# Kernel optimization log

Measured on AMD Instinct MI355X. Metric: run time of the kernel, lower is better.

The kernel has to match this reference:

```python
import jax, jax.numpy as jnp
import numpy as np

EPS_DENOM = 1e-8   # matches probs = counts / (numel + 1e-08)
EPS_LOG = 1e-10    # matches log2(probs + 1e-10)


def setup_inputs() -> dict:
    key = jax.random.key(0)
    values = jax.random.normal(key, (256, 262144), dtype=jnp.float32)
    return {"values": values}


def reference(values):
    # Binary quantization: q = (values > 0). Per batch row, histogram over {0,1}.
    # count1 = number of positives, count0 = N - count1. The torch code's
    # min-shift + bincount over [min..max] yields exactly these counts; the
    # probs[probs>0] filter drops zero-count bins, which contribute 0 anyway
    # (we replicate with jnp.where).
    batch = values.shape[0]
    n = int(np.prod(values.shape[1:]))  # elements per batch row
    q = (values > 0).astype(values.dtype)          # [B, ...]
    count1 = q.reshape(batch, -1).sum(axis=1)      # [B]
    count0 = jnp.asarray(n, values.dtype) - count1 # [B]
    probs = jnp.stack([count0, count1], axis=-1) / (n + EPS_DENOM)  # [B, 2]
    terms = jnp.where(probs > 0, probs * jnp.log2(probs + EPS_LOG), 0.0)
    entropy = -terms.sum(axis=-1)                  # [B]
    return entropy
```

## Files before the change

### kernel.cpp

```cpp
#include <hip/hip_runtime.h>
#include <hip/hip_bf16.h>


#define B_ROWS 256
#define N_PER_ROW 262144
#define BLOCK_THREADS 1024
#define WAVES_PER_BLOCK (BLOCK_THREADS / 64)

__global__ __launch_bounds__(BLOCK_THREADS) void entropy_rows_kernel(
    const float* __restrict__ values, float* __restrict__ out) {
  const int row = blockIdx.x;
  const int tid = threadIdx.x;

  const float4* rowp =
      reinterpret_cast<const float4*>(values + (size_t)row * N_PER_ROW);
  const int n_vec4 = N_PER_ROW / 4;
  const int iters = n_vec4 / BLOCK_THREADS;

  int c = 0;
#pragma unroll 4
  for (int i = 0; i < iters; ++i) {
    float4 v = rowp[(size_t)i * BLOCK_THREADS + tid];
    c += (v.x > 0.0f) + (v.y > 0.0f) + (v.z > 0.0f) + (v.w > 0.0f);
  }

#pragma unroll
  for (int off = 32; off > 0; off >>= 1) c += __shfl_down(c, off, 64);

  __shared__ int wsum[WAVES_PER_BLOCK];
  const int lane = tid & 63;
  const int wave = tid >> 6;
  if (lane == 0) wsum[wave] = c;
  __syncthreads();

  if (tid == 0) {
    int c1 = 0;
#pragma unroll
    for (int w = 0; w < WAVES_PER_BLOCK; ++w) c1 += wsum[w];
    int c0 = N_PER_ROW - c1;
    const float inv_n = 1.0f / (float)N_PER_ROW;
    float p0 = (float)c0 * inv_n;
    float p1 = (float)c1 * inv_n;
    float t0 = (p0 > 0.0f) ? p0 * log2f(p0 + 1e-10f) : 0.0f;
    float t1 = (p1 > 0.0f) ? p1 * log2f(p1 + 1e-10f) : 0.0f;
    out[row] = -(t0 + t1);
  }
}

extern "C" void kernel_launch(void* const* d_in, const int* in_sizes, int n_in,
                              void* d_out, int out_size, void* d_ws, size_t ws_size,
                              hipStream_t stream) {
  const float* values = (const float*)d_in[0];
  float* out = (float*)d_out;
  entropy_rows_kernel<<<B_ROWS, BLOCK_THREADS, 0, stream>>>(values, out);
}
```

Baseline: 53.21 us.

## Split each row across eight blocks and finalize entropy in a second kernel

Each row is now counted by eight 256-thread blocks, giving 2048 blocks in place of 256 one-row blocks, which should fill all CUs on the device and balance memory traffic better. The partial counts go to workspace memory, and a small second kernel sums them and computes the entropy per row. This adds a second launch and depends on the workspace buffer being available.

```diff
diff --git a/kernel.cpp b/kernel.cpp
--- a/kernel.cpp
+++ b/kernel.cpp
@@ -4,23 +4,26 @@
 
 #define B_ROWS 256
 #define N_PER_ROW 262144
-#define BLOCK_THREADS 1024
+#define SLICES 8
+#define SLICE_ELEMS (N_PER_ROW / SLICES)
+#define BLOCK_THREADS 256
 #define WAVES_PER_BLOCK (BLOCK_THREADS / 64)
+#define ITERS (SLICE_ELEMS / 4 / BLOCK_THREADS)
 
-__global__ __launch_bounds__(BLOCK_THREADS) void entropy_rows_kernel(
-    const float* __restrict__ values, float* __restrict__ out) {
-  const int row = blockIdx.x;
+__global__ __launch_bounds__(BLOCK_THREADS) void count_slices_kernel(
+    const float* __restrict__ values, int* __restrict__ partial) {
+  const int blk = blockIdx.x;
+  const int row = blk >> 3;
+  const int slice = blk & (SLICES - 1);
   const int tid = threadIdx.x;
 
-  const float4* rowp =
-      reinterpret_cast<const float4*>(values + (size_t)row * N_PER_ROW);
-  const int n_vec4 = N_PER_ROW / 4;
-  const int iters = n_vec4 / BLOCK_THREADS;
+  const float4* p = reinterpret_cast<const float4*>(
+      values + (size_t)row * N_PER_ROW + (size_t)slice * SLICE_ELEMS);
 
   int c = 0;
-#pragma unroll 4
-  for (int i = 0; i < iters; ++i) {
-    float4 v = rowp[(size_t)i * BLOCK_THREADS + tid];
+#pragma unroll 8
+  for (int i = 0; i < ITERS; ++i) {
+    float4 v = p[i * BLOCK_THREADS + tid];
     c += (v.x > 0.0f) + (v.y > 0.0f) + (v.z > 0.0f) + (v.w > 0.0f);
   }
 
@@ -34,17 +37,26 @@
   __syncthreads();
 
   if (tid == 0) {
-    int c1 = 0;
+    int s = wsum[0];
 #pragma unroll
-    for (int w = 0; w < WAVES_PER_BLOCK; ++w) c1 += wsum[w];
-    int c0 = N_PER_ROW - c1;
-    const float inv_n = 1.0f / (float)N_PER_ROW;
-    float p0 = (float)c0 * inv_n;
-    float p1 = (float)c1 * inv_n;
-    float t0 = (p0 > 0.0f) ? p0 * log2f(p0 + 1e-10f) : 0.0f;
-    float t1 = (p1 > 0.0f) ? p1 * log2f(p1 + 1e-10f) : 0.0f;
-    out[row] = -(t0 + t1);
+    for (int w = 1; w < WAVES_PER_BLOCK; ++w) s += wsum[w];
+    partial[blk] = s;
   }
+}
+
+__global__ __launch_bounds__(B_ROWS) void entropy_finalize_kernel(
+    const int* __restrict__ partial, float* __restrict__ out) {
+  const int row = threadIdx.x;
+  int c1 = 0;
+#pragma unroll
+  for (int s = 0; s < SLICES; ++s) c1 += partial[row * SLICES + s];
+  const int c0 = N_PER_ROW - c1;
+  const float inv_n = 1.0f / (float)N_PER_ROW;
+  const float p0 = (float)c0 * inv_n;
+  const float p1 = (float)c1 * inv_n;
+  const float t0 = (p0 > 0.0f) ? p0 * log2f(p0 + 1e-10f) : 0.0f;
+  const float t1 = (p1 > 0.0f) ? p1 * log2f(p1 + 1e-10f) : 0.0f;
+  out[row] = -(t0 + t1);
 }
 
 extern "C" void kernel_launch(void* const* d_in, const int* in_sizes, int n_in,
@@ -52,5 +64,8 @@
                               hipStream_t stream) {
   const float* values = (const float*)d_in[0];
   float* out = (float*)d_out;
-  entropy_rows_kernel<<<B_ROWS, BLOCK_THREADS, 0, stream>>>(values, out);
+  int* partial = (int*)d_ws;
+
+  count_slices_kernel<<<B_ROWS * SLICES, BLOCK_THREADS, 0, stream>>>(values, partial);
+  entropy_finalize_kernel<<<1, B_ROWS, 0, stream>>>(partial, out);
 }
```

Result: faster. 44.84 us (-15.7%).
